# Kernel optimization log

Measured on AMD Instinct MI355X. Metric: run time of the kernel, lower is better.

The kernel has to match this reference:

```python
import jax, jax.numpy as jnp
import numpy as np

B, IN, HID, EMB, K = 65536, 256, 256, 64, 4096
EPS = 1e-5  # BatchNorm1d default eps


def setup_inputs() -> dict:
    key = jax.random.key(0)
    ks = jax.random.split(key, 12)
    s = 0.05
    return {
        "x": jax.random.normal(ks[0], (B, IN), jnp.float32),
        "W1": jax.random.normal(ks[1], (HID, IN), jnp.float32) * s,
        "b1": jax.random.normal(ks[2], (HID,), jnp.float32) * s,
        "gamma": jnp.ones((HID,), jnp.float32),
        "beta": jnp.zeros((HID,), jnp.float32),
        "mean": jax.random.normal(ks[3], (HID,), jnp.float32) * s,
        "var": jax.random.uniform(ks[4], (HID,), jnp.float32, 0.5, 1.5),
        "W2": jax.random.normal(ks[5], (HID // 2, HID), jnp.float32) * s,
        "b2": jax.random.normal(ks[6], (HID // 2,), jnp.float32) * s,
        "W3": jax.random.normal(ks[7], (EMB, HID // 2), jnp.float32) * s,
        "b3": jax.random.normal(ks[8], (EMB,), jnp.float32) * s,
        "codebook": jax.random.normal(ks[9], (K, EMB), jnp.float32),
    }


def reference(x, W1, b1, gamma, beta, mean, var, W2, b2, W3, b3, codebook):
    # encoder: Linear -> BatchNorm1d (eval stats) -> ReLU -> Linear -> ReLU -> Linear -> Tanh
    h = x @ W1.T + b1                                   # [B, HID]
    h = (h - mean) * jax.lax.rsqrt(var + EPS) * gamma + beta
    h = jax.nn.relu(h)
    h = jax.nn.relu(h @ W2.T + b2)                      # [B, HID//2]
    z = jnp.tanh(h @ W3.T + b3)                         # [B, EMB]
    # squared-distance matrix: ||z||^2 + ||e||^2 - 2 z e^T  -> [B, K]
    d = (jnp.sum(z * z, axis=1, keepdims=True)
         + jnp.sum(codebook * codebook, axis=1)
         - 2.0 * (z @ codebook.T))
    return jnp.argmin(d, axis=1)                        # [B] int token indices
```

## Files before the change

### kernel.cpp

```cpp
#include <hip/hip_runtime.h>

#define IN_DIM  256
#define HID_DIM 256
#define H2_DIM  128
#define EMB_DIM 64
#define K_CODES 4096
#define EPS_BN  1e-5f


typedef _Float16 f16;
typedef _Float16 f16x4 __attribute__((ext_vector_type(4)));
typedef _Float16 f16x8 __attribute__((ext_vector_type(8)));
typedef float    f32x16 __attribute__((ext_vector_type(16)));

__global__ __launch_bounds__(256) void k_norms(const float* __restrict__ cb,
                                               float* __restrict__ norms) {
    int c = blockIdx.x * 256 + threadIdx.x;
    const float4* row = reinterpret_cast<const float4*>(cb + (size_t)c * EMB_DIM);
    float s = 0.f;
#pragma unroll
    for (int i = 0; i < EMB_DIM / 4; ++i) {
        float4 v = row[i];
        s += v.x * v.x + v.y * v.y + v.z * v.z + v.w * v.w;
    }
    norms[c] = 0.5f * s;
}

__global__ __launch_bounds__(256) void k_prep(
    const float* __restrict__ W1, const float* __restrict__ W2,
    const float* __restrict__ W3, const float* __restrict__ cb,
    f16* __restrict__ w1h, f16* __restrict__ w1l,
    f16* __restrict__ w2h, f16* __restrict__ w2l,
    f16* __restrict__ w3h, f16* __restrict__ w3l,
    f16* __restrict__ cbh, f16* __restrict__ cbl) {
    int i = blockIdx.x * 256 + threadIdx.x;
    const float* src; f16 *dh, *dl; int off;
    if (i < 65536)       { src = W1; dh = w1h; dl = w1l; off = i; }
    else if (i < 98304)  { src = W2; dh = w2h; dl = w2l; off = i - 65536; }
    else if (i < 106496) { src = W3; dh = w3h; dl = w3l; off = i - 98304; }
    else                 { src = cb; dh = cbh; dl = cbl; off = i - 106496; }
    float v = src[off];
    f16 h = (f16)v;
    dh[off] = h;
    dl[off] = (f16)(v - (float)h);
}

__global__ __launch_bounds__(256) void k_encoder_mfma(
    const float* __restrict__ x,
    const f16* __restrict__ w1h, const f16* __restrict__ w1l,
    const f16* __restrict__ w2h, const f16* __restrict__ w2l,
    const f16* __restrict__ w3h, const f16* __restrict__ w3l,
    const float* __restrict__ b1,
    const float* __restrict__ gm, const float* __restrict__ bt,
    const float* __restrict__ mu, const float* __restrict__ vr,
    const float* __restrict__ b2, const float* __restrict__ b3,
    f16* __restrict__ Zh, f16* __restrict__ Zl) {
    __shared__ __align__(16) f16 sm[27136];
    const int tid  = threadIdx.x;
    const int lane = tid & 63;
    const int w    = tid >> 6;
    const int ln31 = lane & 31;
    const int q    = lane >> 5;
    const int r0   = blockIdx.x * 32;

    f32x16 acc1a = {};
    f32x16 acc1b = {};
#pragma unroll 1
    for (int kc = 0; kc < 8; ++kc) {
        __syncthreads();
        {
            int row = tid >> 3, c = (tid & 7) * 4;
            float4 v = *reinterpret_cast<const float4*>(
                x + (size_t)(r0 + row) * IN_DIM + kc * 32 + c);
            f16x4 hv, lv;
            hv[0] = (f16)v.x; lv[0] = (f16)(v.x - (float)hv[0]);
            hv[1] = (f16)v.y; lv[1] = (f16)(v.y - (float)hv[1]);
            hv[2] = (f16)v.z; lv[2] = (f16)(v.z - (float)hv[2]);
            hv[3] = (f16)v.w; lv[3] = (f16)(v.w - (float)hv[3]);
            *(f16x4*)(sm + row * 40 + c)        = hv;
            *(f16x4*)(sm + 1280 + row * 40 + c) = lv;
        }
#pragma unroll
        for (int it = 0; it < 4; ++it) {
            int i = it * 256 + tid;
            int j = i >> 2, c8 = (i & 3) * 8;
            *(f16x8*)(sm + 2560 + j * 40 + c8) =
                *(const f16x8*)(w1h + j * IN_DIM + kc * 32 + c8);
            *(f16x8*)(sm + 12800 + j * 40 + c8) =
                *(const f16x8*)(w1l + j * IN_DIM + kc * 32 + c8);
        }
        __syncthreads();
#pragma unroll
        for (int ks = 0; ks < 2; ++ks) {
            f16x8 ah = *(const f16x8*)(sm + ln31 * 40 + ks * 16 + q * 8);
            f16x8 al = *(const f16x8*)(sm + 1280 + ln31 * 40 + ks * 16 + q * 8);
            int j0 = (w * 64 + ln31) * 40 + ks * 16 + q * 8;
            f16x8 bh0 = *(const f16x8*)(sm + 2560 + j0);
            f16x8 bl0 = *(const f16x8*)(sm + 12800 + j0);
            f16x8 bh1 = *(const f16x8*)(sm + 2560 + j0 + 32 * 40);
            f16x8 bl1 = *(const f16x8*)(sm + 12800 + j0 + 32 * 40);
            acc1a = __builtin_amdgcn_mfma_f32_32x32x16_f16(ah, bh0, acc1a, 0, 0, 0);
            acc1b = __builtin_amdgcn_mfma_f32_32x32x16_f16(ah, bh1, acc1b, 0, 0, 0);
            acc1a = __builtin_amdgcn_mfma_f32_32x32x16_f16(al, bh0, acc1a, 0, 0, 0);
            acc1b = __builtin_amdgcn_mfma_f32_32x32x16_f16(al, bh1, acc1b, 0, 0, 0);
            acc1a = __builtin_amdgcn_mfma_f32_32x32x16_f16(ah, bl0, acc1a, 0, 0, 0);
            acc1b = __builtin_amdgcn_mfma_f32_32x32x16_f16(ah, bl1, acc1b, 0, 0, 0);
        }
    }
    __syncthreads();

    {
#pragma unroll
        for (int nt = 0; nt < 2; ++nt) {
            int j = w * 64 + nt * 32 + ln31;
            float sc = gm[j] * rsqrtf(vr[j] + EPS_BN);
            float sh = (b1[j] - mu[j]) * sc + bt[j];
            const f32x16& a = nt ? acc1b : acc1a;
#pragma unroll
            for (int r = 0; r < 16; ++r) {
                int row = (r & 3) + 8 * (r >> 2) + 4 * q;
                float v = a[r] * sc + sh;
                v = v > 0.f ? v : 0.f;
                f16 h = (f16)v;
                sm[row * 264 + j]        = h;
                sm[8448 + row * 264 + j] = (f16)(v - (float)h);
            }
        }
    }

    f32x16 acc2a = {};
    f32x16 acc2b = {};
#pragma unroll 1
    for (int kc = 0; kc < 8; ++kc) {
        __syncthreads();
#pragma unroll
        for (int it = 0; it < 2; ++it) {
            int i = it * 256 + tid;
            int j = i >> 2, c8 = (i & 3) * 8;
            *(f16x8*)(sm + 16896 + j * 40 + c8) =
                *(const f16x8*)(w2h + j * HID_DIM + kc * 32 + c8);
            *(f16x8*)(sm + 22016 + j * 40 + c8) =
                *(const f16x8*)(w2l + j * HID_DIM + kc * 32 + c8);
        }
        __syncthreads();
#pragma unroll
        for (int ks = 0; ks < 2; ++ks) {
            f16x8 ah = *(const f16x8*)(sm + ln31 * 264 + kc * 32 + ks * 16 + q * 8);
            f16x8 al = *(const f16x8*)(sm + 8448 + ln31 * 264 + kc * 32 + ks * 16 + q * 8);
            int j0 = (w * 32 + ln31) * 40 + ks * 16 + q * 8;
            f16x8 bh = *(const f16x8*)(sm + 16896 + j0);
            f16x8 bl = *(const f16x8*)(sm + 22016 + j0);
            f32x16& acc = ks ? acc2b : acc2a;
            acc = __builtin_amdgcn_mfma_f32_32x32x16_f16(ah, bh, acc, 0, 0, 0);
            acc = __builtin_amdgcn_mfma_f32_32x32x16_f16(al, bh, acc, 0, 0, 0);
            acc = __builtin_amdgcn_mfma_f32_32x32x16_f16(ah, bl, acc, 0, 0, 0);
        }
    }
    __syncthreads();

    {
        int j2 = w * 32 + ln31;
        float bias = b2[j2];
#pragma unroll
        for (int r = 0; r < 16; ++r) {
            int row = (r & 3) + 8 * (r >> 2) + 4 * q;
            float v = (acc2a[r] + acc2b[r]) + bias;
            v = v > 0.f ? v : 0.f;
            f16 h = (f16)v;
            sm[row * 136 + j2]        = h;
            sm[4352 + row * 136 + j2] = (f16)(v - (float)h);
        }
#pragma unroll
        for (int it = 0; it < 4; ++it) {
            int i = it * 256 + tid;
            int j = i >> 4, c8 = (i & 15) * 8;
            *(f16x8*)(sm + 8704 + j * 136 + c8) =
                *(const f16x8*)(w3h + j * H2_DIM + c8);
            *(f16x8*)(sm + 17408 + j * 136 + c8) =
                *(const f16x8*)(w3l + j * H2_DIM + c8);
        }
    }
    __syncthreads();

    if (w < 2) {
        f32x16 acc3a = {};
        f32x16 acc3b = {};
#pragma unroll 2
        for (int ks = 0; ks < 8; ++ks) {
            f16x8 ah = *(const f16x8*)(sm + ln31 * 136 + ks * 16 + q * 8);
            f16x8 al = *(const f16x8*)(sm + 4352 + ln31 * 136 + ks * 16 + q * 8);
            int j0 = 8704 + (w * 32 + ln31) * 136 + ks * 16 + q * 8;
            f16x8 bh = *(const f16x8*)(sm + j0);
            f16x8 bl = *(const f16x8*)(sm + j0 + 8704);
            f32x16& acc = (ks & 1) ? acc3b : acc3a;
            acc = __builtin_amdgcn_mfma_f32_32x32x16_f16(ah, bh, acc, 0, 0, 0);
            acc = __builtin_amdgcn_mfma_f32_32x32x16_f16(al, bh, acc, 0, 0, 0);
            acc = __builtin_amdgcn_mfma_f32_32x32x16_f16(ah, bl, acc, 0, 0, 0);
        }
        int j3 = w * 32 + ln31;
        float bias = b3[j3];
#pragma unroll
        for (int r = 0; r < 16; ++r) {
            int row = (r & 3) + 8 * (r >> 2) + 4 * q;
            float zv = tanhf((acc3a[r] + acc3b[r]) + bias);
            f16 h = (f16)zv;
            size_t idx = (size_t)(r0 + row) * EMB_DIM + j3;
            Zh[idx] = h;
            Zl[idx] = (f16)(zv - (float)h);
        }
    }
}

__global__ __launch_bounds__(256) void k_argmin_mfma(
    const f16* __restrict__ Zh, const f16* __restrict__ Zl,
    const f16* __restrict__ cbh, const f16* __restrict__ cbl,
    const float* __restrict__ norms,
    float* __restrict__ part_v, int* __restrict__ part_i) {
    __shared__ __align__(16) f16 sm[18688];
    f16* ebh = sm;
    f16* ebl = sm + 9216;
    float* nbuf = (float*)(sm + 18432);
    const int tid   = threadIdx.x;
    const int lane  = tid & 63;
    const int w     = tid >> 6;
    const int ln31  = lane & 31;
    const int q     = lane >> 5;
    const int r0    = blockIdx.x * 128;
    const int slice = blockIdx.y;

    f16x8 ah[4], al[4];
    {
        const f16* zrh = Zh + (size_t)(r0 + w * 32 + ln31) * EMB_DIM;
        const f16* zrl = Zl + (size_t)(r0 + w * 32 + ln31) * EMB_DIM;
#pragma unroll
        for (int ks = 0; ks < 4; ++ks) {
            ah[ks] = *(const f16x8*)(zrh + ks * 16 + q * 8);
            al[ks] = *(const f16x8*)(zrl + ks * 16 + q * 8);
        }
    }

    float bv[16];
    int   bi[16];
#pragma unroll
    for (int i = 0; i < 16; ++i) { bv[i] = -3.4e38f; bi[i] = 0; }

    for (int ch = slice * 8; ch < slice * 8 + 8; ++ch) {
        __syncthreads();
        const float4* srch = (const float4*)(cbh + (size_t)ch * 128 * EMB_DIM);
        const float4* srcl = (const float4*)(cbl + (size_t)ch * 128 * EMB_DIM);
        float4* dsth = (float4*)ebh;
        float4* dstl = (float4*)ebl;
#pragma unroll
        for (int it = 0; it < 4; ++it) {
            int i = it * 256 + tid;
            int row = i >> 3, c8 = i & 7;
            dsth[row * 9 + c8] = srch[row * 8 + c8];
            dstl[row * 9 + c8] = srcl[row * 8 + c8];
        }
        if (tid < 128) nbuf[tid] = norms[ch * 128 + tid];
        __syncthreads();

#pragma unroll 1
        for (int ct = 0; ct < 4; ++ct) {
            f16x8 bh[4], bl[4];
#pragma unroll
            for (int ks = 0; ks < 4; ++ks) {
                int off = (ct * 32 + ln31) * 72 + ks * 16 + q * 8;
                bh[ks] = *(const f16x8*)(ebh + off);
                bl[ks] = *(const f16x8*)(ebl + off);
            }
            f32x16 acc0 = {};
            f32x16 acc1 = {};
#pragma unroll
            for (int ks = 0; ks < 4; ks += 2) {
                acc0 = __builtin_amdgcn_mfma_f32_32x32x16_f16(ah[ks],     bh[ks],     acc0, 0, 0, 0);
                acc1 = __builtin_amdgcn_mfma_f32_32x32x16_f16(ah[ks + 1], bh[ks + 1], acc1, 0, 0, 0);
                acc0 = __builtin_amdgcn_mfma_f32_32x32x16_f16(al[ks],     bh[ks],     acc0, 0, 0, 0);
                acc1 = __builtin_amdgcn_mfma_f32_32x32x16_f16(al[ks + 1], bh[ks + 1], acc1, 0, 0, 0);
                acc0 = __builtin_amdgcn_mfma_f32_32x32x16_f16(ah[ks],     bl[ks],     acc0, 0, 0, 0);
                acc1 = __builtin_amdgcn_mfma_f32_32x32x16_f16(ah[ks + 1], bl[ks + 1], acc1, 0, 0, 0);
            }
            float nv  = nbuf[ct * 32 + ln31];
            int   col = ch * 128 + ct * 32 + ln31;
#pragma unroll
            for (int r = 0; r < 16; ++r) {
                float t  = (acc0[r] + acc1[r]) - nv;
                bool  gt = t > bv[r];
                bv[r] = gt ? t : bv[r];
                bi[r] = gt ? col : bi[r];
            }
        }
    }

    __syncthreads();
    float* redv = (float*)sm;
    int*   redi = (int*)(sm + 8448);
#pragma unroll
    for (int r = 0; r < 16; ++r) {
        int row = (r & 3) + 8 * (r >> 2) + 4 * q + 32 * w;
        redv[row * 33 + ln31] = bv[r];
        redi[row * 33 + ln31] = bi[r];
    }
    __syncthreads();
    if (tid < 128) {
        float v  = redv[tid * 33];
        int   ix = redi[tid * 33];
#pragma unroll
        for (int j = 1; j < 32; ++j) {
            float vj = redv[tid * 33 + j];
            int   ij = redi[tid * 33 + j];
            if (vj > v) { v = vj; ix = ij; }
        }
        int r = r0 + tid;
        part_v[(size_t)r * 4 + slice] = v;
        part_i[(size_t)r * 4 + slice] = ix;
    }
}

__global__ __launch_bounds__(256) void k_merge(const float* __restrict__ part_v,
                                               const int* __restrict__ part_i,
                                               int* __restrict__ out) {
    int r = blockIdx.x * 256 + threadIdx.x;
    float4 pv = *reinterpret_cast<const float4*>(part_v + (size_t)r * 4);
    int4   pi = *reinterpret_cast<const int4*>(part_i + (size_t)r * 4);
    float v = pv.x; int ix = pi.x;
    if (pv.y > v) { v = pv.y; ix = pi.y; }
    if (pv.z > v) { v = pv.z; ix = pi.z; }
    if (pv.w > v) { v = pv.w; ix = pi.w; }
    out[r] = ix;
}

extern "C" void kernel_launch(void* const* d_in, const int* in_sizes, int n_in,
                              void* d_out, int out_size, void* d_ws, size_t ws_size,
                              hipStream_t stream) {
    (void)n_in; (void)out_size; (void)ws_size;
    const float* x  = (const float*)d_in[0];
    const float* W1 = (const float*)d_in[1];
    const float* b1 = (const float*)d_in[2];
    const float* gm = (const float*)d_in[3];
    const float* bt = (const float*)d_in[4];
    const float* mu = (const float*)d_in[5];
    const float* vr = (const float*)d_in[6];
    const float* W2 = (const float*)d_in[7];
    const float* b2 = (const float*)d_in[8];
    const float* W3 = (const float*)d_in[9];
    const float* b3 = (const float*)d_in[10];
    const float* cb = (const float*)d_in[11];

    char* ws = (char*)d_ws;
    float* norms = (float*)ws;
    f16* cbh = (f16*)(ws + 16384);
    f16* cbl = (f16*)(ws + 540672);
    f16* w1h = (f16*)(ws + 1064960);
    f16* w1l = (f16*)(ws + 1196032);
    f16* w2h = (f16*)(ws + 1327104);
    f16* w2l = (f16*)(ws + 1392640);
    f16* w3h = (f16*)(ws + 1458176);
    f16* w3l = (f16*)(ws + 1474560);
    f16* Zh  = (f16*)(ws + 1490944);
    f16* Zl  = (f16*)(ws + 9879552);
    float* part_v = (float*)(ws + 18268160);
    int*   part_i = (int*)(ws + 19316736);
    int* out = (int*)d_out;

    const int B = in_sizes[0] / IN_DIM;

    k_norms<<<K_CODES / 256, 256, 0, stream>>>(cb, norms);
    k_prep<<<1440, 256, 0, stream>>>(W1, W2, W3, cb, w1h, w1l, w2h, w2l,
                                     w3h, w3l, cbh, cbl);
    k_encoder_mfma<<<B / 32, 256, 0, stream>>>(x, w1h, w1l, w2h, w2l, w3h, w3l,
                                               b1, gm, bt, mu, vr, b2, b3, Zh, Zl);
    dim3 ag(B / 128, 4);
    k_argmin_mfma<<<ag, 256, 0, stream>>>(Zh, Zl, cbh, cbl, norms, part_v, part_i);
    k_merge<<<B / 256, 256, 0, stream>>>(part_v, part_i, out);
}
```

Measured before the change: 296.8 us.

## Read encoder weights directly from global memory instead of staging through LDS

The encoder kernel no longer copies W1/W2/W3 hi/lo tiles into shared memory each k-chunk. Each lane now loads its MFMA B operand straight from global memory, which the L2 is expected to serve since the weights are shared by all blocks. The 32-row x tile is staged in LDS once up front rather than per chunk. This removes most __syncthreads barriers and cuts LDS from about 54KB to 34KB, raising possible occupancy, at the cost of uncoalesced per-lane global loads on the MFMA critical path.

New measurement: 320.9 us. 1.08x slower.

```diff
diff --git a/kernel.cpp b/kernel.cpp
--- a/kernel.cpp
+++ b/kernel.cpp
@@ -55,7 +55,7 @@
     const float* __restrict__ mu, const float* __restrict__ vr,
     const float* __restrict__ b2, const float* __restrict__ b3,
     f16* __restrict__ Zh, f16* __restrict__ Zl) {
-    __shared__ __align__(16) f16 sm[27136];
+    __shared__ __align__(16) f16 sm[16896];
     const int tid  = threadIdx.x;
     const int lane = tid & 63;
     const int w    = tid >> 6;
@@ -63,97 +63,86 @@
     const int q    = lane >> 5;
     const int r0   = blockIdx.x * 32;
 
+#pragma unroll
+    for (int it = 0; it < 8; ++it) {
+        int i = it * 256 + tid;
+        int row = i >> 6, c4 = i & 63;
+        float4 v = *reinterpret_cast<const float4*>(
+            x + (size_t)(r0 + row) * IN_DIM + c4 * 4);
+        f16x4 hv, lv;
+        hv[0] = (f16)v.x; lv[0] = (f16)(v.x - (float)hv[0]);
+        hv[1] = (f16)v.y; lv[1] = (f16)(v.y - (float)hv[1]);
+        hv[2] = (f16)v.z; lv[2] = (f16)(v.z - (float)hv[2]);
+        hv[3] = (f16)v.w; lv[3] = (f16)(v.w - (float)hv[3]);
+        *(f16x4*)(sm + row * 264 + c4 * 4)        = hv;
+        *(f16x4*)(sm + 8448 + row * 264 + c4 * 4) = lv;
+    }
+    __syncthreads();
+
     f32x16 acc1a = {};
     f32x16 acc1b = {};
+    {
+        const f16* p1h = w1h + (w * 64 + ln31) * IN_DIM + q * 8;
+        const f16* p1l = w1l + (w * 64 + ln31) * IN_DIM + q * 8;
 #pragma unroll 1
-    for (int kc = 0; kc < 8; ++kc) {
-        __syncthreads();
-        {
-            int row = tid >> 3, c = (tid & 7) * 4;
-            float4 v = *reinterpret_cast<const float4*>(
-                x + (size_t)(r0 + row) * IN_DIM + kc * 32 + c);
-            f16x4 hv, lv;
-            hv[0] = (f16)v.x; lv[0] = (f16)(v.x - (float)hv[0]);
-            hv[1] = (f16)v.y; lv[1] = (f16)(v.y - (float)hv[1]);
-            hv[2] = (f16)v.z; lv[2] = (f16)(v.z - (float)hv[2]);
-            hv[3] = (f16)v.w; lv[3] = (f16)(v.w - (float)hv[3]);
-            *(f16x4*)(sm + row * 40 + c)        = hv;
-            *(f16x4*)(sm + 1280 + row * 40 + c) = lv;
-        }
-#pragma unroll
-        for (int it = 0; it < 4; ++it) {
-            int i = it * 256 + tid;
-            int j = i >> 2, c8 = (i & 3) * 8;
-            *(f16x8*)(sm + 2560 + j * 40 + c8) =
-                *(const f16x8*)(w1h + j * IN_DIM + kc * 32 + c8);
-            *(f16x8*)(sm + 12800 + j * 40 + c8) =
-                *(const f16x8*)(w1l + j * IN_DIM + kc * 32 + c8);
-        }
-        __syncthreads();
-#pragma unroll
-        for (int ks = 0; ks < 2; ++ks) {
-            f16x8 ah = *(const f16x8*)(sm + ln31 * 40 + ks * 16 + q * 8);
-            f16x8 al = *(const f16x8*)(sm + 1280 + ln31 * 40 + ks * 16 + q * 8);
-            int j0 = (w * 64 + ln31) * 40 + ks * 16 + q * 8;
-            f16x8 bh0 = *(const f16x8*)(sm + 2560 + j0);
-            f16x8 bl0 = *(const f16x8*)(sm + 12800 + j0);
-            f16x8 bh1 = *(const f16x8*)(sm + 2560 + j0 + 32 * 40);
-            f16x8 bl1 = *(const f16x8*)(sm + 12800 + j0 + 32 * 40);
-            acc1a = __builtin_amdgcn_mfma_f32_32x32x16_f16(ah, bh0, acc1a, 0, 0, 0);
-            acc1b = __builtin_amdgcn_mfma_f32_32x32x16_f16(ah, bh1, acc1b, 0, 0, 0);
-            acc1a = __builtin_amdgcn_mfma_f32_32x32x16_f16(al, bh0, acc1a, 0, 0, 0);
-            acc1b = __builtin_amdgcn_mfma_f32_32x32x16_f16(al, bh1, acc1b, 0, 0, 0);
-            acc1a = __builtin_amdgcn_mfma_f32_32x32x16_f16(ah, bl0, acc1a, 0, 0, 0);
-            acc1b = __builtin_amdgcn_mfma_f32_32x32x16_f16(ah, bl1, acc1b, 0, 0, 0);
-        }
-    }
-    __syncthreads();
-
-    {
-#pragma unroll
-        for (int nt = 0; nt < 2; ++nt) {
-            int j = w * 64 + nt * 32 + ln31;
-            float sc = gm[j] * rsqrtf(vr[j] + EPS_BN);
-            float sh = (b1[j] - mu[j]) * sc + bt[j];
-            const f32x16& a = nt ? acc1b : acc1a;
-#pragma unroll
-            for (int r = 0; r < 16; ++r) {
-                int row = (r & 3) + 8 * (r >> 2) + 4 * q;
-                float v = a[r] * sc + sh;
-                v = v > 0.f ? v : 0.f;
-                f16 h = (f16)v;
-                sm[row * 264 + j]        = h;
-                sm[8448 + row * 264 + j] = (f16)(v - (float)h);
-            }
-        }
-    }
+        for (int kc = 0; kc < 8; ++kc) {
+#pragma unroll
+            for (int ks = 0; ks < 2; ++ks) {
+                int ko = kc * 32 + ks * 16;
+                f16x8 ah  = *(const f16x8*)(sm + ln31 * 264 + ko + q * 8);
+                f16x8 al  = *(const f16x8*)(sm + 8448 + ln31 * 264 + ko + q * 8);
+                f16x8 bh0 = *(const f16x8*)(p1h + ko);
+                f16x8 bl0 = *(const f16x8*)(p1l + ko);
+                f16x8 bh1 = *(const f16x8*)(p1h + 32 * IN_DIM + ko);
+                f16x8 bl1 = *(const f16x8*)(p1l + 32 * IN_DIM + ko);
+                acc1a = __builtin_amdgcn_mfma_f32_32x32x16_f16(ah, bh0, acc1a, 0, 0, 0);
+                acc1b = __builtin_amdgcn_mfma_f32_32x32x16_f16(ah, bh1, acc1b, 0, 0, 0);
+                acc1a = __builtin_amdgcn_mfma_f32_32x32x16_f16(al, bh0, acc1a, 0, 0, 0);
+                acc1b = __builtin_amdgcn_mfma_f32_32x32x16_f16(al, bh1, acc1b, 0, 0, 0);
+                acc1a = __builtin_amdgcn_mfma_f32_32x32x16_f16(ah, bl0, acc1a, 0, 0, 0);
+                acc1b = __builtin_amdgcn_mfma_f32_32x32x16_f16(ah, bl1, acc1b, 0, 0, 0);
+            }
+        }
+    }
+    __syncthreads();
+
+#pragma unroll
+    for (int nt = 0; nt < 2; ++nt) {
+        int j = w * 64 + nt * 32 + ln31;
+        float sc = gm[j] * rsqrtf(vr[j] + EPS_BN);
+        float sh = (b1[j] - mu[j]) * sc + bt[j];
+        const f32x16& a = nt ? acc1b : acc1a;
+#pragma unroll
+        for (int r = 0; r < 16; ++r) {
+            int row = (r & 3) + 8 * (r >> 2) + 4 * q;
+            float v = a[r] * sc + sh;
+            v = v > 0.f ? v : 0.f;
+            f16 h = (f16)v;
+            sm[row * 264 + j]        = h;
+            sm[8448 + row * 264 + j] = (f16)(v - (float)h);
+        }
+    }
+    __syncthreads();
 
     f32x16 acc2a = {};
     f32x16 acc2b = {};
+    {
+        const f16* p2h = w2h + (w * 32 + ln31) * HID_DIM + q * 8;
+        const f16* p2l = w2l + (w * 32 + ln31) * HID_DIM + q * 8;
 #pragma unroll 1
-    for (int kc = 0; kc < 8; ++kc) {
-        __syncthreads();
-#pragma unroll
-        for (int it = 0; it < 2; ++it) {
-            int i = it * 256 + tid;
-            int j = i >> 2, c8 = (i & 3) * 8;
-            *(f16x8*)(sm + 16896 + j * 40 + c8) =
-                *(const f16x8*)(w2h + j * HID_DIM + kc * 32 + c8);
-            *(f16x8*)(sm + 22016 + j * 40 + c8) =
-                *(const f16x8*)(w2l + j * HID_DIM + kc * 32 + c8);
-        }
-        __syncthreads();
-#pragma unroll
-        for (int ks = 0; ks < 2; ++ks) {
-            f16x8 ah = *(const f16x8*)(sm + ln31 * 264 + kc * 32 + ks * 16 + q * 8);
-            f16x8 al = *(const f16x8*)(sm + 8448 + ln31 * 264 + kc * 32 + ks * 16 + q * 8);
-            int j0 = (w * 32 + ln31) * 40 + ks * 16 + q * 8;
-            f16x8 bh = *(const f16x8*)(sm + 16896 + j0);
-            f16x8 bl = *(const f16x8*)(sm + 22016 + j0);
-            f32x16& acc = ks ? acc2b : acc2a;
-            acc = __builtin_amdgcn_mfma_f32_32x32x16_f16(ah, bh, acc, 0, 0, 0);
-            acc = __builtin_amdgcn_mfma_f32_32x32x16_f16(al, bh, acc, 0, 0, 0);
-            acc = __builtin_amdgcn_mfma_f32_32x32x16_f16(ah, bl, acc, 0, 0, 0);
+        for (int kc = 0; kc < 8; ++kc) {
+#pragma unroll
+            for (int ks = 0; ks < 2; ++ks) {
+                int ko = kc * 32 + ks * 16;
+                f16x8 ah = *(const f16x8*)(sm + ln31 * 264 + ko + q * 8);
+                f16x8 al = *(const f16x8*)(sm + 8448 + ln31 * 264 + ko + q * 8);
+                f16x8 bh = *(const f16x8*)(p2h + ko);
+                f16x8 bl = *(const f16x8*)(p2l + ko);
+                f32x16& acc = ks ? acc2b : acc2a;
+                acc = __builtin_amdgcn_mfma_f32_32x32x16_f16(ah, bh, acc, 0, 0, 0);
+                acc = __builtin_amdgcn_mfma_f32_32x32x16_f16(al, bh, acc, 0, 0, 0);
+                acc = __builtin_amdgcn_mfma_f32_32x32x16_f16(ah, bl, acc, 0, 0, 0);
+            }
         }
     }
     __syncthreads();
@@ -170,28 +159,20 @@
             sm[row * 136 + j2]        = h;
             sm[4352 + row * 136 + j2] = (f16)(v - (float)h);
         }
-#pragma unroll
-        for (int it = 0; it < 4; ++it) {
-            int i = it * 256 + tid;
-            int j = i >> 4, c8 = (i & 15) * 8;
-            *(f16x8*)(sm + 8704 + j * 136 + c8) =
-                *(const f16x8*)(w3h + j * H2_DIM + c8);
-            *(f16x8*)(sm + 17408 + j * 136 + c8) =
-                *(const f16x8*)(w3l + j * H2_DIM + c8);
-        }
     }
     __syncthreads();
 
     if (w < 2) {
         f32x16 acc3a = {};
         f32x16 acc3b = {};
+        const f16* p3h = w3h + (w * 32 + ln31) * H2_DIM + q * 8;
+        const f16* p3l = w3l + (w * 32 + ln31) * H2_DIM + q * 8;
 #pragma unroll 2
         for (int ks = 0; ks < 8; ++ks) {
             f16x8 ah = *(const f16x8*)(sm + ln31 * 136 + ks * 16 + q * 8);
             f16x8 al = *(const f16x8*)(sm + 4352 + ln31 * 136 + ks * 16 + q * 8);
-            int j0 = 8704 + (w * 32 + ln31) * 136 + ks * 16 + q * 8;
-            f16x8 bh = *(const f16x8*)(sm + j0);
-            f16x8 bl = *(const f16x8*)(sm + j0 + 8704);
+            f16x8 bh = *(const f16x8*)(p3h + ks * 16);
+            f16x8 bl = *(const f16x8*)(p3l + ks * 16);
             f32x16& acc = (ks & 1) ? acc3b : acc3a;
             acc = __builtin_amdgcn_mfma_f32_32x32x16_f16(ah, bh, acc, 0, 0, 0);
             acc = __builtin_amdgcn_mfma_f32_32x32x16_f16(al, bh, acc, 0, 0, 0);
```
